# Kernel tuning notes

Hardware: AMD Instinct MI355X
Metric: run time of the kernel (lower is better)

## Reference

```python
import jax, jax.numpy as jnp
import numpy as np

N = 2048       # num nodes
E = 4096       # num edges
D_NODE = 128
D_EDGE = 128
H = 4          # heads
DH = D_EDGE // H
C = 16         # num classes
NODE_K = N // 2   # node_k_ratio = 0.5
EDGE_K = E // 2   # edge_k_ratio = 0.5
NEG = -1e9


def setup_inputs() -> dict:
    key = jax.random.key(0)
    ks = jax.random.split(key, 16)
    w = lambda k, shape: jax.random.normal(k, shape, jnp.float32) * 0.02
    return {
        "node_features": jax.random.normal(ks[0], (N, D_NODE), jnp.float32),
        "edge_features": jax.random.normal(ks[1], (E, D_EDGE), jnp.float32),
        "edge_index": jax.random.randint(ks[2], (2, E), 0, N, jnp.int32),
        # ImportanceRouter: scalar scores per node / edge
        "w_router_n": w(ks[3], (D_NODE,)),
        "w_router_e": w(ks[4], (D_EDGE,)),
        # EdgeAttention projections
        "w_e": w(ks[5], (D_EDGE, D_EDGE)),
        "w_n": w(ks[6], (D_NODE, D_EDGE)),
        "w_q": w(ks[7], (D_EDGE, D_EDGE)),
        "w_k": w(ks[8], (D_EDGE, D_EDGE)),
        "w_v": w(ks[9], (D_EDGE, D_EDGE)),
        "w_o": w(ks[10], (D_EDGE, D_EDGE)),
        # classifier MLP: Linear -> GELU -> Linear
        "w1": w(ks[11], (D_EDGE, D_EDGE)),
        "b1": jnp.zeros((D_EDGE,), jnp.float32),
        "w2": w(ks[12], (D_EDGE, C)),
        "b2": jnp.zeros((C,), jnp.float32),
    }


def reference(node_features, edge_features, edge_index,
              w_router_n, w_router_e,
              w_e, w_n, w_q, w_k, w_v, w_o,
              w1, b1, w2, b2):
    src, dst = edge_index[0], edge_index[1]

    # --- ImportanceRouter: node/edge scores ---
    ns = node_features @ w_router_n   # [N]
    es = edge_features @ w_router_e   # [E]

    # --- apply_top_k(node_k_ratio=0.5, edge_k_ratio=0.5) ---
    _, nidx = jax.lax.top_k(ns, NODE_K)
    node_mask = jnp.zeros((N,), bool).at[nidx].set(True)
    _, eidx = jax.lax.top_k(es, EDGE_K)
    edge_topk = jnp.zeros((E,), bool).at[eidx].set(True)
    edge_mask = edge_topk & node_mask[src] & node_mask[dst]   # [E]

    ef = edge_features * edge_mask[:, None].astype(edge_features.dtype)

    # --- build_edge_adjacency: edges sharing a node attend to each other ---
    adj = ((src[:, None] == src[None, :]) | (src[:, None] == dst[None, :]) |
           (dst[:, None] == src[None, :]) | (dst[:, None] == dst[None, :]))  # [E,E]

    # --- EdgeAttention: edge rep mixes edge feats and endpoint node feats ---
    h = ef @ w_e + (node_features[src] + node_features[dst]) @ w_n   # [E, D_EDGE]
    q = (h @ w_q).reshape(E, H, DH)
    k = (h @ w_k).reshape(E, H, DH)
    v = (h @ w_v).reshape(E, H, DH)
    scores = jnp.einsum('ehd,fhd->hef', q, k) / np.float32(np.sqrt(DH))  # [H,E,E]
    scores = jnp.where(adj[None, :, :], scores, NEG)
    attn = jax.nn.softmax(scores, axis=-1)
    o = jnp.einsum('hef,fhd->ehd', attn, v).reshape(E, D_EDGE) @ w_o    # [E, D_EDGE]

    # --- classifier: Linear -> GELU -> Linear ---
    x = jax.nn.gelu(o @ w1 + b1)
    logits = x @ w2 + b2            # [E, C]
    return logits
```

## Files before the change

### kernel.cpp

```cpp
#include <hip/hip_runtime.h>
#include <hip/hip_bf16.h>
#include <math.h>

#define NN 2048
#define NE 4096
#define D 128
#define NODE_K 1024
#define EDGE_K 2048
#define CAP 64

typedef const __hip_bfloat16* bfp;
typedef unsigned short u16;
typedef __attribute__((ext_vector_type(8))) short short8;
typedef __attribute__((ext_vector_type(4))) float floatx4;

#define MFMA16(a, b, c) __builtin_amdgcn_mfma_f32_16x16x32_bf16(a, b, c, 0, 0, 0)

__device__ __forceinline__ float b2f(__hip_bfloat16 x) { return __bfloat162float(x); }

__device__ __forceinline__ float ldx(const void* p, size_t i, int f) {
  return f ? ((const float*)p)[i] : b2f(((bfp)p)[i]);
}
__device__ __forceinline__ float4 ldx4(const void* p, size_t i4, int f) {
  if (f) return ((const float4*)p)[i4];
  ushort4 u = ((const ushort4*)p)[i4];
  float4 r;
  r.x = __uint_as_float(((unsigned)u.x) << 16);
  r.y = __uint_as_float(((unsigned)u.y) << 16);
  r.z = __uint_as_float(((unsigned)u.z) << 16);
  r.w = __uint_as_float(((unsigned)u.w) << 16);
  return r;
}

__device__ __forceinline__ void split2(float x, u16& hi, u16& lo) {
  unsigned u = __float_as_uint(x);
  unsigned h = (u + 0x7FFFu + ((u >> 16) & 1u)) >> 16;
  hi = (u16)h;
  float r = x - __uint_as_float(h << 16);
  unsigned v = __float_as_uint(r);
  lo = (u16)((v + 0x7FFFu + ((v >> 16) & 1u)) >> 16);
}
__device__ __forceinline__ void build_frags(const float* v8, short8& fh, short8& fl) {
  #pragma unroll
  for (int i = 0; i < 8; ++i) {
    u16 h, l;
    split2(v8[i], h, l);
    fh[i] = (short)h; fl[i] = (short)l;
  }
}

template <int NT>
__device__ __forceinline__ int detect_f(const u16* raw, int* s8) {
  int t = threadIdx.x;
  int weird = 0;
  for (int i = t; i < 1024; i += NT) {
    unsigned int bits = ((unsigned int)raw[i]) << 16;
    float x = __uint_as_float(bits);
    float ax = fabsf(x);
    if (!(ax <= 1e3f) || (x != 0.f && ax < 1e-12f)) weird++;
  }
  #pragma unroll
  for (int m = 32; m >= 1; m >>= 1) weird += __shfl_xor(weird, m);
  if ((t & 63) == 0) s8[t >> 6] = weird;
  __syncthreads();
  int tot = 0;
  #pragma unroll
  for (int i = 0; i < NT / 64; ++i) tot += s8[i];
  return (tot > 50) ? 1 : 0;
}

struct K1Args {
  const void *nf, *ef, *wrn, *wre;
  const void* w[7];
  const int *src, *dst;
  float *ns, *es;
  int *deg, *lists, *flag;
  u16 *wtHi, *wtLo;
  u16 *feHi, *feLo;
};

#define SCORE_BLOCKS ((NN + NE) / 4)
#define WPREP_BLOCKS 112
#define FSPLIT_BLOCKS 192
#define K1_BLOCKS (SCORE_BLOCKS + WPREP_BLOCKS + FSPLIT_BLOCKS + 1)
__global__ __launch_bounds__(256) void scores_prep_lists_kernel(K1Args a) {
  __shared__ int s8[4];
  int b = blockIdx.x, t = threadIdx.x;
  int f = detect_f<256>((const u16*)a.nf, s8);
  if (b < SCORE_BLOCKS) {
    int wid = b * 4 + (t >> 6), lane = t & 63;
    const void* base; const void* w; float* out; size_t r0;
    if (wid < NN) { base = a.nf; r0 = (size_t)wid * D; w = a.wrn; out = a.ns + wid; }
    else { int r = wid - NN; base = a.ef; r0 = (size_t)r * D; w = a.wre; out = a.es + r; }
    double p = (double)ldx(base, r0 + lane, f) * (double)ldx(w, lane, f)
             + (double)ldx(base, r0 + lane + 64, f) * (double)ldx(w, lane + 64, f);
    #pragma unroll
    for (int m = 32; m >= 1; m >>= 1) p += __shfl_xor(p, m);
    if (lane == 0) *out = (float)p;
  } else if (b < SCORE_BLOCKS + WPREP_BLOCKS) {
    int tau = (b - SCORE_BLOCKS) * 256 + t;
    int w = tau >> 12, rem = tau & 4095;
    int n = rem >> 5, k0 = (rem & 31) * 4;
    ushort4 hi, lo;
    split2(ldx(a.w[w], (size_t)(k0 + 0) * 128 + n, f), hi.x, lo.x);
    split2(ldx(a.w[w], (size_t)(k0 + 1) * 128 + n, f), hi.y, lo.y);
    split2(ldx(a.w[w], (size_t)(k0 + 2) * 128 + n, f), hi.z, lo.z);
    split2(ldx(a.w[w], (size_t)(k0 + 3) * 128 + n, f), hi.w, lo.w);
    ((ushort4*)a.wtHi)[tau] = hi;
    ((ushort4*)a.wtLo)[tau] = lo;
  } else if (b < SCORE_BLOCKS + WPREP_BLOCKS + FSPLIT_BLOCKS) {
    int fb = b - SCORE_BLOCKS - WPREP_BLOCKS;
    #pragma unroll
    for (int i = 0; i < 4; ++i) {
      int g4 = fb * 1024 + i * 256 + t;
      float4 x = (g4 < NN * D / 4) ? ldx4(a.nf, g4, f)
                                   : ldx4(a.ef, g4 - NN * D / 4, f);
      ushort4 hi, lo;
      split2(x.x, hi.x, lo.x);
      split2(x.y, hi.y, lo.y);
      split2(x.z, hi.z, lo.z);
      split2(x.w, hi.w, lo.w);
      ((ushort4*)a.feHi)[g4] = hi;
      ((ushort4*)a.feLo)[g4] = lo;
    }
  } else {
    __shared__ int ldeg[NN];
    for (int i = t; i < NN; i += 256) ldeg[i] = 0;
    __syncthreads();
    #pragma unroll
    for (int i = 0; i < NE / 256; ++i) {
      int e = i * 256 + t;
      int sn = a.src[e], dn = a.dst[e];
      int p = atomicAdd(&ldeg[sn], 1);
      if (p < CAP) a.lists[sn * CAP + p] = e;
      if (dn != sn) {
        p = atomicAdd(&ldeg[dn], 1);
        if (p < CAP) a.lists[dn * CAP + p] = e;
      }
    }
    __syncthreads();
    for (int i = t; i < NN; i += 256) a.deg[i] = ldeg[i];
    if (t == 0) a.flag[0] = f;
  }
}

__global__ __launch_bounds__(512) void h_qkv_mfma_kernel(
    const float* __restrict__ ns, const float* __restrict__ es,
    const u16* __restrict__ feHi, const u16* __restrict__ feLo,
    const int* __restrict__ src, const int* __restrict__ dst,
    const u16* __restrict__ wtHi, const u16* __restrict__ wtLo,
    float* __restrict__ qkv) {
  __shared__ __align__(16) float hf[8 * 64 * 4];
  __shared__ int s_msk[3][16];
  int t = threadIdx.x;
  int wave = t >> 6, lane = t & 63;
  int qd = lane >> 4, c = lane & 15;
  int row0 = blockIdx.x * 16;

  for (int task = wave; task < 48; task += 8) {
    int kind = task >> 4, ti = task & 15;
    int e2 = row0 + ti;
    const float* arr; int len, K, tgt;
    if (kind == 0) { arr = es; len = NE; K = EDGE_K; tgt = e2; }
    else { arr = ns; len = NN; K = NODE_K; tgt = (kind == 1) ? src[e2] : dst[e2]; }
    float si = arr[tgt];
    int rank = 0;
    for (int j4 = lane; j4 < (len >> 2); j4 += 64) {
      float4 sj = ((const float4*)arr)[j4];
      int j = j4 * 4;
      rank += (sj.x > si) || (sj.x == si && j + 0 < tgt);
      rank += (sj.y > si) || (sj.y == si && j + 1 < tgt);
      rank += (sj.z > si) || (sj.z == si && j + 2 < tgt);
      rank += (sj.w > si) || (sj.w == si && j + 3 < tgt);
    }
    #pragma unroll
    for (int m = 32; m >= 1; m >>= 1) rank += __shfl_xor(rank, m);
    if (lane == 0) s_msk[kind][ti] = (rank < K) ? 1 : 0;
  }
  __syncthreads();

  int e = row0 + c;
  int sn = src[e], dn = dst[e];
  bool em = s_msk[0][c] && s_msk[1][c] && s_msk[2][c];
  int n0 = wave * 16;
  const u16* efH = feHi + (size_t)NN * D;
  const u16* efL = feLo + (size_t)NN * D;
  const short8 z8 = {0, 0, 0, 0, 0, 0, 0, 0};

  short8 A1h[4], A1l[4], Sh[4], Sl[4], Dh[4], Dl[4];
  short8 BEh[4], BEl[4], BNh[4], BNl[4];
  #pragma unroll
  for (int ks = 0; ks < 4; ++ks) {
    int k0 = ks * 32 + qd * 8;
    A1h[ks] = *(const short8*)(efH + (size_t)e * D + k0);
    A1l[ks] = *(const short8*)(efL + (size_t)e * D + k0);
    Sh[ks]  = *(const short8*)(feHi + (size_t)sn * D + k0);
    Sl[ks]  = *(const short8*)(feLo + (size_t)sn * D + k0);
    Dh[ks]  = *(const short8*)(feHi + (size_t)dn * D + k0);
    Dl[ks]  = *(const short8*)(feLo + (size_t)dn * D + k0);
    size_t bo = (size_t)(n0 + c) * 128 + k0;
    BEh[ks] = *(const short8*)(wtHi + bo);
    BEl[ks] = *(const short8*)(wtLo + bo);
    BNh[ks] = *(const short8*)(wtHi + 16384 + bo);
    BNl[ks] = *(const short8*)(wtLo + 16384 + bo);
  }
  if (!em) {
    #pragma unroll
    for (int ks = 0; ks < 4; ++ks) { A1h[ks] = z8; A1l[ks] = z8; }
  }
  floatx4 accE = {0.f, 0.f, 0.f, 0.f};
  floatx4 accN = {0.f, 0.f, 0.f, 0.f};
  #pragma unroll
  for (int ks = 0; ks < 4; ++ks) {
    accE = MFMA16(A1h[ks], BEh[ks], accE);
    accN = MFMA16(Sh[ks], BNh[ks], accN);
    accE = MFMA16(A1l[ks], BEh[ks], accE);
    accN = MFMA16(Sl[ks], BNh[ks], accN);
    accE = MFMA16(A1h[ks], BEl[ks], accE);
    accN = MFMA16(Sh[ks], BNl[ks], accN);
    accN = MFMA16(Dh[ks], BNh[ks], accN);
    accN = MFMA16(Dl[ks], BNh[ks], accN);
    accN = MFMA16(Dh[ks], BNl[ks], accN);
  }
  {
    int np = n0 + c;
    int kd = np >> 5, qq = (np >> 3) & 3, half = (c >> 2) & 1, j4 = c & 3;
    #pragma unroll
    for (int r = 0; r < 4; ++r)
      hf[((kd * 2 + half) * 64 + qq * 16 + 4 * qd + r) * 4 + j4] = accE[r] + accN[r];
  }
  short8 BQh[4], BQl[4], BKh[4], BKl[4], BVh[4], BVl[4];
  #pragma unroll
  for (int ks = 0; ks < 4; ++ks) {
    size_t bo = (size_t)(n0 + c) * 128 + ks * 32 + qd * 8;
    BQh[ks] = *(const short8*)(wtHi + 2 * 16384 + bo);
    BQl[ks] = *(const short8*)(wtLo + 2 * 16384 + bo);
    BKh[ks] = *(const short8*)(wtHi + 3 * 16384 + bo);
    BKl[ks] = *(const short8*)(wtLo + 3 * 16384 + bo);
    BVh[ks] = *(const short8*)(wtHi + 4 * 16384 + bo);
    BVl[ks] = *(const short8*)(wtLo + 4 * 16384 + bo);
  }
  __syncthreads();
  floatx4 aq = {0.f, 0.f, 0.f, 0.f};
  floatx4 ak = {0.f, 0.f, 0.f, 0.f};
  floatx4 av = {0.f, 0.f, 0.f, 0.f};
  #pragma unroll
  for (int ks = 0; ks < 4; ++ks) {
    float4 p0 = *(const float4*)&hf[((ks * 2 + 0) * 64 + lane) * 4];
    float4 p1 = *(const float4*)&hf[((ks * 2 + 1) * 64 + lane) * 4];
    float v8[8] = {p0.x, p0.y, p0.z, p0.w, p1.x, p1.y, p1.z, p1.w};
    short8 ah, al;
    build_frags(v8, ah, al);
    aq = MFMA16(ah, BQh[ks], aq);
    ak = MFMA16(ah, BKh[ks], ak);
    av = MFMA16(ah, BVh[ks], av);
    aq = MFMA16(al, BQh[ks], aq);
    ak = MFMA16(al, BKh[ks], ak);
    av = MFMA16(al, BVh[ks], av);
    aq = MFMA16(ah, BQl[ks], aq);
    ak = MFMA16(ah, BKl[ks], ak);
    av = MFMA16(ah, BVl[ks], av);
  }
  #pragma unroll
  for (int r = 0; r < 4; ++r) {
    size_t ro = (size_t)(row0 + 4 * qd + r) * D + n0 + c;
    qkv[ro] = aq[r];
    qkv[(size_t)NE * D + ro] = ak[r];
    qkv[(size_t)2 * NE * D + ro] = av[r];
  }
}

__global__ __launch_bounds__(1024) void attn_mlp_kernel(
    const float* __restrict__ qkv, const int* __restrict__ src,
    const int* __restrict__ dst, const int* __restrict__ deg,
    const int* __restrict__ lists,
    const u16* __restrict__ wtHi, const u16* __restrict__ wtLo,
    const void* __restrict__ b1, const void* __restrict__ w2,
    const void* __restrict__ b2, const int* __restrict__ flag,
    void* __restrict__ out) {
  __shared__ __align__(16) float ao_lds[16 * 132];
  __shared__ __align__(16) float hf[8 * 64 * 4];
  __shared__ __align__(16) float xl[16 * 132];
  __shared__ __align__(16) float w2t[16 * 132];
  int t = threadIdx.x;
  int wave = t >> 6, lane = t & 63;
  int row0 = blockIdx.x * 16;

  {
    const float* qb = qkv;
    const float* kb = qkv + (size_t)NE * D;
    const float* vb = qkv + (size_t)2 * NE * D;
    int half = lane >> 5, l5 = lane & 31;
    int d0 = l5 + 64 * half;
    int d1 = d0 + 32;
    int e = row0 + wave;
    int sn = src[e], dn = dst[e];
    const float scale = 0.17677669529663687f;
    float q0 = qb[(size_t)e * D + d0], q1 = qb[(size_t)e * D + d1];
    float m0 = -1e30f, l0 = 0.f, a0 = 0.f;
    float m1 = -1e30f, l1 = 0.f, a1 = 0.f;
    int degA = max(0, min(deg[sn], CAP));
    for (int i = 0; i < degA; ++i) {
      int fe = lists[sn * CAP + i];
      float p0 = q0 * kb[(size_t)fe * D + d0];
      float p1 = q1 * kb[(size_t)fe * D + d1];
      #pragma unroll
      for (int mk = 16; mk >= 1; mk >>= 1) {
        p0 += __shfl_xor(p0, mk);
        p1 += __shfl_xor(p1, mk);
      }
      float v0 = vb[(size_t)fe * D + d0], v1 = vb[(size_t)fe * D + d1];
      float s0 = p0 * scale, s1 = p1 * scale;
      float n0_ = fmaxf(m0, s0), n1_ = fmaxf(m1, s1);
      float c0 = expf(m0 - n0_), c1 = expf(m1 - n1_);
      float w0 = expf(s0 - n0_), w1 = expf(s1 - n1_);
      l0 = l0 * c0 + w0; a0 = a0 * c0 + w0 * v0; m0 = n0_;
      l1 = l1 * c1 + w1; a1 = a1 * c1 + w1 * v1; m1 = n1_;
    }
    if (dn != sn) {
      int degB = max(0, min(deg[dn], CAP));
      for (int i = 0; i < degB; ++i) {
        int fe = lists[dn * CAP + i];
        if (src[fe] == sn || dst[fe] == sn) continue;
        float p0 = q0 * kb[(size_t)fe * D + d0];
        float p1 = q1 * kb[(size_t)fe * D + d1];
        #pragma unroll
        for (int mk = 16; mk >= 1; mk >>= 1) {
          p0 += __shfl_xor(p0, mk);
          p1 += __shfl_xor(p1, mk);
        }
        float v0 = vb[(size_t)fe * D + d0], v1 = vb[(size_t)fe * D + d1];
        float s0 = p0 * scale, s1 = p1 * scale;
        float n0_ = fmaxf(m0, s0), n1_ = fmaxf(m1, s1);
        float c0 = expf(m0 - n0_), c1 = expf(m1 - n1_);
        float w0 = expf(s0 - n0_), w1 = expf(s1 - n1_);
        l0 = l0 * c0 + w0; a0 = a0 * c0 + w0 * v0; m0 = n0_;
        l1 = l1 * c1 + w1; a1 = a1 * c1 + w1 * v1; m1 = n1_;
      }
    }
    ao_lds[wave * 132 + d0] = a0 / fmaxf(l0, 1e-37f);
    ao_lds[wave * 132 + d1] = a1 / fmaxf(l1, 1e-37f);
  }
  __syncthreads();

  int f = flag[0];
  int qd = lane >> 4, c = lane & 15;
  int n0 = wave * 16;
  if (t < 512) {
    short8 BOh[4], BOl[4], B1h[4], B1l[4];
    #pragma unroll
    for (int ks = 0; ks < 4; ++ks) {
      size_t bo = (size_t)(n0 + c) * 128 + ks * 32 + qd * 8;
      BOh[ks] = *(const short8*)(wtHi + 5 * 16384 + bo);
      BOl[ks] = *(const short8*)(wtLo + 5 * 16384 + bo);
      B1h[ks] = *(const short8*)(wtHi + 6 * 16384 + bo);
      B1l[ks] = *(const short8*)(wtLo + 6 * 16384 + bo);
    }
    floatx4 acc = {0.f, 0.f, 0.f, 0.f};
    #pragma unroll
    for (int ks = 0; ks < 4; ++ks) {
      int k0 = ks * 32 + qd * 8;
      const float* ap = &ao_lds[c * 132 + k0];
      float4 p0 = *(const float4*)ap;
      float4 p1 = *(const float4*)(ap + 4);
      float v8[8] = {p0.x, p0.y, p0.z, p0.w, p1.x, p1.y, p1.z, p1.w};
      short8 ah, al;
      build_frags(v8, ah, al);
      acc = MFMA16(ah, BOh[ks], acc);
      acc = MFMA16(al, BOh[ks], acc);
      acc = MFMA16(ah, BOl[ks], acc);
    }
    {
      int np = n0 + c;
      int kd = np >> 5, qq = (np >> 3) & 3, half = (c >> 2) & 1, j4 = c & 3;
      #pragma unroll
      for (int r = 0; r < 4; ++r)
        hf[((kd * 2 + half) * 64 + qq * 16 + 4 * qd + r) * 4 + j4] = acc[r];
    }
    __syncthreads();
    floatx4 a2c = {0.f, 0.f, 0.f, 0.f};
    #pragma unroll
    for (int ks = 0; ks < 4; ++ks) {
      float4 p0 = *(const float4*)&hf[((ks * 2 + 0) * 64 + lane) * 4];
      float4 p1 = *(const float4*)&hf[((ks * 2 + 1) * 64 + lane) * 4];
      float v8[8] = {p0.x, p0.y, p0.z, p0.w, p1.x, p1.y, p1.z, p1.w};
      short8 ah, al;
      build_frags(v8, ah, al);
      a2c = MFMA16(ah, B1h[ks], a2c);
      a2c = MFMA16(al, B1h[ks], a2c);
      a2c = MFMA16(ah, B1l[ks], a2c);
    }
    float bj = ldx(b1, n0 + c, f);
    #pragma unroll
    for (int r = 0; r < 4; ++r) {
      float u = a2c[r] + bj;
      float inner = 0.7978845608028654f * (u + 0.044715f * u * u * u);
      xl[(4 * qd + r) * 132 + n0 + c] = 0.5f * u * (1.f + tanhf(inner));
    }
  } else {
    for (int i = t - 512; i < D * 16; i += 512) {
      int kk = i >> 4, cc = i & 15;
      w2t[cc * 132 + kk] = ldx(w2, i, f);
    }
    __syncthreads();
  }
  __syncthreads();
  if (t < 256) {
    int r = t >> 4, cc = t & 15;
    const float4* xr = (const float4*)&xl[r * 132];
    const float4* wr = (const float4*)&w2t[cc * 132];
    float s = 0.f;
    #pragma unroll
    for (int k4 = 0; k4 < D / 4; ++k4) {
      float4 xa = xr[k4], wb = wr[k4];
      s += xa.x * wb.x + xa.y * wb.y + xa.z * wb.z + xa.w * wb.w;
    }
    s += ldx(b2, cc, f);
    int idx = (row0 + r) * 16 + cc;
    if (f) ((float*)out)[idx] = s;
    else ((__hip_bfloat16*)out)[idx] = __float2bfloat16(s);
  }
}

extern "C" void kernel_launch(void* const* d_in, const int* in_sizes, int n_in,
                              void* d_out, int out_size, void* d_ws, size_t ws_size,
                              hipStream_t stream) {
  const int* eidx = (const int*)d_in[2];
  const int* src = eidx;
  const int* dst = eidx + NE;

  size_t off = 0;
  char* base = (char*)d_ws;
  auto alloc = [&](size_t nbytes) -> void* {
    void* p = base + off;
    off += (nbytes + 255) & ~(size_t)255;
    return p;
  };
  int* flag      = (int*)alloc(256);
  float* ns      = (float*)alloc(NN * sizeof(float));
  float* es      = (float*)alloc(NE * sizeof(float));
  int* deg       = (int*)alloc(NN * sizeof(int));
  int* lists     = (int*)alloc((size_t)NN * CAP * sizeof(int));
  u16* wtHi      = (u16*)alloc((size_t)7 * 16384 * sizeof(u16));
  u16* wtLo      = (u16*)alloc((size_t)7 * 16384 * sizeof(u16));
  u16* feHi      = (u16*)alloc((size_t)(NN + NE) * D * sizeof(u16));
  u16* feLo      = (u16*)alloc((size_t)(NN + NE) * D * sizeof(u16));
  float* qkv     = (float*)alloc((size_t)3 * NE * D * sizeof(float));
  float* qb = qkv, *kb = qkv + NE * D, *vb = qkv + 2 * NE * D;
  (void)qb; (void)kb; (void)vb;

  K1Args a1;
  a1.nf = d_in[0]; a1.ef = d_in[1]; a1.wrn = d_in[3]; a1.wre = d_in[4];
  a1.w[0] = d_in[5];  a1.w[1] = d_in[6];  a1.w[2] = d_in[7];
  a1.w[3] = d_in[8];  a1.w[4] = d_in[9];  a1.w[5] = d_in[10]; a1.w[6] = d_in[11];
  a1.src = src; a1.dst = dst;
  a1.ns = ns; a1.es = es; a1.deg = deg; a1.lists = lists; a1.flag = flag;
  a1.wtHi = wtHi; a1.wtLo = wtLo; a1.feHi = feHi; a1.feLo = feLo;

  scores_prep_lists_kernel<<<K1_BLOCKS, 256, 0, stream>>>(a1);
  h_qkv_mfma_kernel<<<NE / 16, 512, 0, stream>>>(
      ns, es, feHi, feLo, src, dst, wtHi, wtLo, qkv);
  attn_mlp_kernel<<<NE / 16, 1024, 0, stream>>>(
      qkv, src, dst, deg, lists, wtHi, wtLo,
      d_in[12], d_in[13], d_in[14], flag, d_out);
}
```

Before: 161.0 us.

## Split sparse attention into per-edge kernel with two-pass softmax and separate MLP kernel

Replaces the fused attention+MLP kernel with two kernels. The new attention kernel gives each edge its own 256-thread block, gathers the neighbour list into shared memory with a ballot-compacted dedup, computes scores across waves, and runs a two-pass softmax before a weighted V sum. This removes the serial per-edge online-softmax loop with long dependent chains. The cost is an extra global round trip for the attention output and one more kernel launch.

New measurement: 150.4 us. -6.6%, faster.

```diff
diff --git a/kernel.cpp b/kernel.cpp
--- a/kernel.cpp
+++ b/kernel.cpp
@@ -270,139 +270,149 @@
   }
 }
 
-__global__ __launch_bounds__(1024) void attn_mlp_kernel(
+__global__ __launch_bounds__(256) void attn_kernel(
     const float* __restrict__ qkv, const int* __restrict__ src,
     const int* __restrict__ dst, const int* __restrict__ deg,
-    const int* __restrict__ lists,
+    const int* __restrict__ lists, float* __restrict__ ao) {
+  __shared__ int nb[2 * CAP];
+  __shared__ float sS[4][2 * CAP];
+  __shared__ float inv_l[4];
+  __shared__ int sM;
+  const float* kb = qkv + (size_t)NE * D;
+  const float* vb = qkv + (size_t)2 * NE * D;
+  int e = blockIdx.x;
+  int t = threadIdx.x;
+  int wave = t >> 6, lane = t & 63;
+  int sn = src[e], dn = dst[e];
+  float2 qv = *(const float2*)&qkv[(size_t)e * D + 2 * lane];
+  int degA = max(0, min(deg[sn], CAP));
+  int degB = (dn != sn) ? max(0, min(deg[dn], CAP)) : 0;
+  if (wave == 0) {
+    if (lane < degA) nb[lane] = lists[sn * CAP + lane];
+  } else if (wave == 1) {
+    int fe = -1;
+    bool keep = false;
+    if (lane < degB) {
+      fe = lists[dn * CAP + lane];
+      keep = !(src[fe] == sn || dst[fe] == sn);
+    }
+    unsigned long long mk = __ballot(keep);
+    if (keep) {
+      int pos = __popcll(mk & ((1ULL << lane) - 1ULL));
+      nb[degA + pos] = fe;
+    }
+    if (lane == 0) sM = degA + __popcll(mk);
+  }
+  __syncthreads();
+  int M = sM;
+  const float scale = 0.17677669529663687f;
+  for (int i = wave; i < M; i += 4) {
+    int fe = nb[i];
+    float2 kk = *(const float2*)&kb[(size_t)fe * D + 2 * lane];
+    float p = qv.x * kk.x + qv.y * kk.y;
+    p += __shfl_xor(p, 8); p += __shfl_xor(p, 4);
+    p += __shfl_xor(p, 2); p += __shfl_xor(p, 1);
+    if ((lane & 15) == 0) sS[lane >> 4][i] = p * scale;
+  }
+  __syncthreads();
+  {
+    float mx = -1e30f;
+    for (int i = lane; i < M; i += 64) mx = fmaxf(mx, sS[wave][i]);
+    #pragma unroll
+    for (int mk2 = 32; mk2 >= 1; mk2 >>= 1) mx = fmaxf(mx, __shfl_xor(mx, mk2));
+    float ls = 0.f;
+    for (int i = lane; i < M; i += 64) {
+      float w = expf(sS[wave][i] - mx);
+      sS[wave][i] = w;
+      ls += w;
+    }
+    #pragma unroll
+    for (int mk2 = 32; mk2 >= 1; mk2 >>= 1) ls += __shfl_xor(ls, mk2);
+    if (lane == 0) inv_l[wave] = 1.f / fmaxf(ls, 1e-37f);
+  }
+  __syncthreads();
+  if (t < D) {
+    int h = t >> 5;
+    float acc0 = 0.f, acc1 = 0.f;
+    int i = 0;
+    for (; i + 1 < M; i += 2) {
+      acc0 += sS[h][i]     * vb[(size_t)nb[i] * D + t];
+      acc1 += sS[h][i + 1] * vb[(size_t)nb[i + 1] * D + t];
+    }
+    if (i < M) acc0 += sS[h][i] * vb[(size_t)nb[i] * D + t];
+    ao[(size_t)e * D + t] = (acc0 + acc1) * inv_l[h];
+  }
+}
+
+__global__ __launch_bounds__(512) void o_mlp_mfma_kernel(
+    const float* __restrict__ ao,
     const u16* __restrict__ wtHi, const u16* __restrict__ wtLo,
     const void* __restrict__ b1, const void* __restrict__ w2,
     const void* __restrict__ b2, const int* __restrict__ flag,
     void* __restrict__ out) {
-  __shared__ __align__(16) float ao_lds[16 * 132];
   __shared__ __align__(16) float hf[8 * 64 * 4];
   __shared__ __align__(16) float xl[16 * 132];
   __shared__ __align__(16) float w2t[16 * 132];
   int t = threadIdx.x;
   int wave = t >> 6, lane = t & 63;
+  int qd = lane >> 4, c = lane & 15;
+  int f = flag[0];
   int row0 = blockIdx.x * 16;
-
+  int n0 = wave * 16;
+
+  short8 BOh[4], BOl[4], B1h[4], B1l[4];
+  #pragma unroll
+  for (int ks = 0; ks < 4; ++ks) {
+    size_t bo = (size_t)(n0 + c) * 128 + ks * 32 + qd * 8;
+    BOh[ks] = *(const short8*)(wtHi + 5 * 16384 + bo);
+    BOl[ks] = *(const short8*)(wtLo + 5 * 16384 + bo);
+    B1h[ks] = *(const short8*)(wtHi + 6 * 16384 + bo);
+    B1l[ks] = *(const short8*)(wtLo + 6 * 16384 + bo);
+  }
+  floatx4 acc = {0.f, 0.f, 0.f, 0.f};
+  #pragma unroll
+  for (int ks = 0; ks < 4; ++ks) {
+    int k0 = ks * 32 + qd * 8;
+    const float* ap = ao + (size_t)(row0 + c) * D + k0;
+    float4 p0 = *(const float4*)ap;
+    float4 p1 = *(const float4*)(ap + 4);
+    float v8[8] = {p0.x, p0.y, p0.z, p0.w, p1.x, p1.y, p1.z, p1.w};
+    short8 ah, al;
+    build_frags(v8, ah, al);
+    acc = MFMA16(ah, BOh[ks], acc);
+    acc = MFMA16(al, BOh[ks], acc);
+    acc = MFMA16(ah, BOl[ks], acc);
+  }
   {
-    const float* qb = qkv;
-    const float* kb = qkv + (size_t)NE * D;
-    const float* vb = qkv + (size_t)2 * NE * D;
-    int half = lane >> 5, l5 = lane & 31;
-    int d0 = l5 + 64 * half;
-    int d1 = d0 + 32;
-    int e = row0 + wave;
-    int sn = src[e], dn = dst[e];
-    const float scale = 0.17677669529663687f;
-    float q0 = qb[(size_t)e * D + d0], q1 = qb[(size_t)e * D + d1];
-    float m0 = -1e30f, l0 = 0.f, a0 = 0.f;
-    float m1 = -1e30f, l1 = 0.f, a1 = 0.f;
-    int degA = max(0, min(deg[sn], CAP));
-    for (int i = 0; i < degA; ++i) {
-      int fe = lists[sn * CAP + i];
-      float p0 = q0 * kb[(size_t)fe * D + d0];
-      float p1 = q1 * kb[(size_t)fe * D + d1];
-      #pragma unroll
-      for (int mk = 16; mk >= 1; mk >>= 1) {
-        p0 += __shfl_xor(p0, mk);
-        p1 += __shfl_xor(p1, mk);
-      }
-      float v0 = vb[(size_t)fe * D + d0], v1 = vb[(size_t)fe * D + d1];
-      float s0 = p0 * scale, s1 = p1 * scale;
-      float n0_ = fmaxf(m0, s0), n1_ = fmaxf(m1, s1);
-      float c0 = expf(m0 - n0_), c1 = expf(m1 - n1_);
-      float w0 = expf(s0 - n0_), w1 = expf(s1 - n1_);
-      l0 = l0 * c0 + w0; a0 = a0 * c0 + w0 * v0; m0 = n0_;
-      l1 = l1 * c1 + w1; a1 = a1 * c1 + w1 * v1; m1 = n1_;
-    }
-    if (dn != sn) {
-      int degB = max(0, min(deg[dn], CAP));
-      for (int i = 0; i < degB; ++i) {
-        int fe = lists[dn * CAP + i];
-        if (src[fe] == sn || dst[fe] == sn) continue;
-        float p0 = q0 * kb[(size_t)fe * D + d0];
-        float p1 = q1 * kb[(size_t)fe * D + d1];
-        #pragma unroll
-        for (int mk = 16; mk >= 1; mk >>= 1) {
-          p0 += __shfl_xor(p0, mk);
-          p1 += __shfl_xor(p1, mk);
-        }
-        float v0 = vb[(size_t)fe * D + d0], v1 = vb[(size_t)fe * D + d1];
-        float s0 = p0 * scale, s1 = p1 * scale;
-        float n0_ = fmaxf(m0, s0), n1_ = fmaxf(m1, s1);
-        float c0 = expf(m0 - n0_), c1 = expf(m1 - n1_);
-        float w0 = expf(s0 - n0_), w1 = expf(s1 - n1_);
-        l0 = l0 * c0 + w0; a0 = a0 * c0 + w0 * v0; m0 = n0_;
-        l1 = l1 * c1 + w1; a1 = a1 * c1 + w1 * v1; m1 = n1_;
-      }
-    }
-    ao_lds[wave * 132 + d0] = a0 / fmaxf(l0, 1e-37f);
-    ao_lds[wave * 132 + d1] = a1 / fmaxf(l1, 1e-37f);
-  }
-  __syncthreads();
-
-  int f = flag[0];
-  int qd = lane >> 4, c = lane & 15;
-  int n0 = wave * 16;
-  if (t < 512) {
-    short8 BOh[4], BOl[4], B1h[4], B1l[4];
-    #pragma unroll
-    for (int ks = 0; ks < 4; ++ks) {
-      size_t bo = (size_t)(n0 + c) * 128 + ks * 32 + qd * 8;
-      BOh[ks] = *(const short8*)(wtHi + 5 * 16384 + bo);
-      BOl[ks] = *(const short8*)(wtLo + 5 * 16384 + bo);
-      B1h[ks] = *(const short8*)(wtHi + 6 * 16384 + bo);
-      B1l[ks] = *(const short8*)(wtLo + 6 * 16384 + bo);
-    }
-    floatx4 acc = {0.f, 0.f, 0.f, 0.f};
-    #pragma unroll
-    for (int ks = 0; ks < 4; ++ks) {
-      int k0 = ks * 32 + qd * 8;
-      const float* ap = &ao_lds[c * 132 + k0];
-      float4 p0 = *(const float4*)ap;
-      float4 p1 = *(const float4*)(ap + 4);
-      float v8[8] = {p0.x, p0.y, p0.z, p0.w, p1.x, p1.y, p1.z, p1.w};
-      short8 ah, al;
-      build_frags(v8, ah, al);
-      acc = MFMA16(ah, BOh[ks], acc);
-      acc = MFMA16(al, BOh[ks], acc);
-      acc = MFMA16(ah, BOl[ks], acc);
-    }
-    {
-      int np = n0 + c;
-      int kd = np >> 5, qq = (np >> 3) & 3, half = (c >> 2) & 1, j4 = c & 3;
-      #pragma unroll
-      for (int r = 0; r < 4; ++r)
-        hf[((kd * 2 + half) * 64 + qq * 16 + 4 * qd + r) * 4 + j4] = acc[r];
-    }
-    __syncthreads();
-    floatx4 a2c = {0.f, 0.f, 0.f, 0.f};
-    #pragma unroll
-    for (int ks = 0; ks < 4; ++ks) {
-      float4 p0 = *(const float4*)&hf[((ks * 2 + 0) * 64 + lane) * 4];
-      float4 p1 = *(const float4*)&hf[((ks * 2 + 1) * 64 + lane) * 4];
-      float v8[8] = {p0.x, p0.y, p0.z, p0.w, p1.x, p1.y, p1.z, p1.w};
-      short8 ah, al;
-      build_frags(v8, ah, al);
-      a2c = MFMA16(ah, B1h[ks], a2c);
-      a2c = MFMA16(al, B1h[ks], a2c);
-      a2c = MFMA16(ah, B1l[ks], a2c);
-    }
-    float bj = ldx(b1, n0 + c, f);
-    #pragma unroll
-    for (int r = 0; r < 4; ++r) {
-      float u = a2c[r] + bj;
-      float inner = 0.7978845608028654f * (u + 0.044715f * u * u * u);
-      xl[(4 * qd + r) * 132 + n0 + c] = 0.5f * u * (1.f + tanhf(inner));
-    }
-  } else {
-    for (int i = t - 512; i < D * 16; i += 512) {
-      int kk = i >> 4, cc = i & 15;
-      w2t[cc * 132 + kk] = ldx(w2, i, f);
-    }
-    __syncthreads();
+    int np = n0 + c;
+    int kd = np >> 5, qq = (np >> 3) & 3, half = (c >> 2) & 1, j4 = c & 3;
+    #pragma unroll
+    for (int r = 0; r < 4; ++r)
+      hf[((kd * 2 + half) * 64 + qq * 16 + 4 * qd + r) * 4 + j4] = acc[r];
+  }
+  __syncthreads();
+  floatx4 a2c = {0.f, 0.f, 0.f, 0.f};
+  #pragma unroll
+  for (int ks = 0; ks < 4; ++ks) {
+    float4 p0 = *(const float4*)&hf[((ks * 2 + 0) * 64 + lane) * 4];
+    float4 p1 = *(const float4*)&hf[((ks * 2 + 1) * 64 + lane) * 4];
+    float v8[8] = {p0.x, p0.y, p0.z, p0.w, p1.x, p1.y, p1.z, p1.w};
+    short8 ah, al;
+    build_frags(v8, ah, al);
+    a2c = MFMA16(ah, B1h[ks], a2c);
+    a2c = MFMA16(al, B1h[ks], a2c);
+    a2c = MFMA16(ah, B1l[ks], a2c);
+  }
+  float bj = ldx(b1, n0 + c, f);
+  #pragma unroll
+  for (int r = 0; r < 4; ++r) {
+    float u = a2c[r] + bj;
+    float inner = 0.7978845608028654f * (u + 0.044715f * u * u * u);
+    xl[(4 * qd + r) * 132 + n0 + c] = 0.5f * u * (1.f + tanhf(inner));
+  }
+  for (int i = t; i < D * 16; i += 512) {
+    int kk = i >> 4, cc = i & 15;
+    w2t[cc * 132 + kk] = ldx(w2, i, f);
   }
   __syncthreads();
   if (t < 256) {
@@ -446,8 +456,7 @@
   u16* feHi      = (u16*)alloc((size_t)(NN + NE) * D * sizeof(u16));
   u16* feLo      = (u16*)alloc((size_t)(NN + NE) * D * sizeof(u16));
   float* qkv     = (float*)alloc((size_t)3 * NE * D * sizeof(float));
-  float* qb = qkv, *kb = qkv + NE * D, *vb = qkv + 2 * NE * D;
-  (void)qb; (void)kb; (void)vb;
+  float* ao      = (float*)alloc((size_t)NE * D * sizeof(float));
 
   K1Args a1;
   a1.nf = d_in[0]; a1.ef = d_in[1]; a1.wrn = d_in[3]; a1.wre = d_in[4];
@@ -460,7 +469,7 @@
   scores_prep_lists_kernel<<<K1_BLOCKS, 256, 0, stream>>>(a1);
   h_qkv_mfma_kernel<<<NE / 16, 512, 0, stream>>>(
       ns, es, feHi, feLo, src, dst, wtHi, wtLo, qkv);
-  attn_mlp_kernel<<<NE / 16, 1024, 0, stream>>>(
-      qkv, src, dst, deg, lists, wtHi, wtLo,
-      d_in[12], d_in[13], d_in[14], flag, d_out);
-}
+  attn_kernel<<<NE, 256, 0, stream>>>(qkv, src, dst, deg, lists, ao);
+  o_mlp_mfma_kernel<<<NE / 16, 512, 0, stream>>>(
+      ao, wtHi, wtLo, d_in[12], d_in[13], d_in[14], flag, d_out);
+}
```
